# Kernel optimization log

Hardware: AMD Instinct MI355X
Metric: run time of the kernel (lower is better)

Reference implementation:

```python
import jax, jax.numpy as jnp
import numpy as np

B, T, E = 4, 2048, 1024
H, D = 16, 64  # num_heads, head_size; H*D == E


def setup_inputs() -> dict:
    key = jax.random.key(0)
    ks = jax.random.split(key, 8)
    s = 0.02
    x = jax.random.normal(ks[0], (B, T, E), dtype=jnp.float32)
    attention_mask = jnp.ones((B, T), dtype=jnp.float32)
    # stacked per-head projection weights (no bias), torch Linear: y = x @ W.T
    Wq = jax.random.normal(ks[1], (H, E, D), dtype=jnp.float32) * s
    Wk = jax.random.normal(ks[2], (H, E, D), dtype=jnp.float32) * s
    Wv = jax.random.normal(ks[3], (H, E, D), dtype=jnp.float32) * s
    Wo = jax.random.normal(ks[4], (E, E), dtype=jnp.float32) * s
    bo = jnp.zeros((E,), dtype=jnp.float32)
    return {"x": x, "attention_mask": attention_mask, "Wq": Wq, "Wk": Wk,
            "Wv": Wv, "Wo": Wo, "bo": bo}


def reference(x, attention_mask, Wq, Wk, Wv, Wo, bo):
    # per-head projections, vectorized over heads: [B,T,E] x [H,E,D] -> [B,H,T,D]
    q = jnp.einsum('bte,hed->bhtd', x, Wq)
    k = jnp.einsum('bte,hed->bhtd', x, Wk)
    v = jnp.einsum('bte,hed->bhtd', x, Wv)
    scores = jnp.einsum('bhtd,bhsd->bhts', q, k) / jnp.sqrt(jnp.float32(D))
    # causal mask (tril): masked_fill with -inf
    causal = jnp.tril(jnp.ones((T, T), dtype=bool))
    scores = jnp.where(causal[None, None, :, :], scores, -jnp.inf)
    # padding mask: weights += (1 - mask) * finfo(float32).min, broadcast over queries
    neg = jnp.finfo(jnp.float32).min
    scores = scores + ((1.0 - attention_mask) * neg)[:, None, None, :]
    weights = jax.nn.softmax(scores, axis=-1)
    out = jnp.einsum('bhts,bhsd->bthd', weights, v).reshape(B, T, H * D)
    return out @ Wo.T + bo
```

## Files before the change

### kernel.cpp

```cpp
#include <hip/hip_runtime.h>
#include <hip/hip_bf16.h>

#define B_ 4
#define T_ 2048
#define E_ 1024
#define H_ 16
#define D_ 64
#define M_ (B_*T_)

typedef short bf16x8 __attribute__((ext_vector_type(8)));
typedef float f32x4  __attribute__((ext_vector_type(4)));
typedef float f32x16 __attribute__((ext_vector_type(16)));

__device__ __forceinline__ short f2bf(float f) {
    __hip_bfloat16 h = __float2bfloat16(f);
    return *reinterpret_cast<short*>(&h);
}

__device__ __forceinline__ void async_ld16(const void* g, void* l) {
    __builtin_amdgcn_global_load_lds(
        (const __attribute__((address_space(1))) unsigned int*)g,
        (__attribute__((address_space(3))) unsigned int*)l, 16, 0, 0);
}

__global__ __launch_bounds__(256) void prep_fused(
        const float* __restrict__ x,   const float* __restrict__ Wo,
        const float* __restrict__ Wq,  const float* __restrict__ Wk,
        const float* __restrict__ Wv,  const float* __restrict__ mask,
        short* __restrict__ xb, short* __restrict__ Wob,
        short* __restrict__ Wt, float* __restrict__ bias) {
    __shared__ float tile[64][65];
    const int bi  = blockIdx.x;
    const int tid = threadIdx.x;

    if (bi < 9216) {
        const float* src = (bi < 8192) ? x : Wo;
        short* dst       = (bi < 8192) ? xb : Wob;
        const int i = ((bi < 8192) ? bi : (bi - 8192)) * 256 + tid;
        float4 v = ((const float4*)src)[i];
        short4 o = make_short4(f2bf(v.x), f2bf(v.y), f2bf(v.z), f2bf(v.w));
        ((short4*)dst)[i] = o;
    } else if (bi < 9984) {
        const int idx = bi - 9216;
        const int which = idx >> 8;
        const int h  = (idx & 255) >> 4;
        const int e0 = (idx & 15) * 64;
        const float* __restrict__ W = (which == 0) ? Wq : (which == 1) ? Wk : Wv;
#pragma unroll
        for (int r = 0; r < 4; ++r) {
            int lin = tid + r * 256;
            int er = lin >> 4, c4 = (lin & 15) * 4;
            float4 v = *(const float4*)(W + ((size_t)h * E_ + e0 + er) * D_ + c4);
            tile[er][c4 + 0] = v.x; tile[er][c4 + 1] = v.y;
            tile[er][c4 + 2] = v.z; tile[er][c4 + 3] = v.w;
        }
        __syncthreads();
#pragma unroll
        for (int r = 0; r < 4; ++r) {
            int lin = tid + r * 256;
            int dr = lin >> 4, j4 = (lin & 15) * 4;
            short4 o = make_short4(f2bf(tile[j4 + 0][dr]), f2bf(tile[j4 + 1][dr]),
                                   f2bf(tile[j4 + 2][dr]), f2bf(tile[j4 + 3][dr]));
            *(short4*)(Wt + ((size_t)which * 1024 + h * 64 + dr) * E_ + e0 + j4) = o;
        }
    } else {
        const int i = (bi - 9984) * 256 + tid;
        float bm = (1.0f - mask[i]) * -3.402823466e38f;
        bias[i] = fmaf(bm, 1.4426950f, -8.6561700f);
    }
}

template <int MODE>
__global__ __launch_bounds__(512, 4) void mfma_gemm(
        const short* __restrict__ A,
        const short* __restrict__ Bt,
        short* __restrict__ qo, short* __restrict__ ko, short* __restrict__ vo,
        float* __restrict__ Cout, const float* __restrict__ bo) {
    __shared__ __align__(16) char lds[3 * 24576];

    const int tid  = threadIdx.x;
    const int wave = tid >> 6, lane = tid & 63;
    const int c = lane & 15, quad = lane >> 4;
    const int wm = wave >> 1, wn = wave & 1;
    const int m0 = blockIdx.x * 256;
    const int n0 = blockIdx.y * 128;

    const int ar = tid >> 2;
    const int ag = (tid & 3) ^ ((tid >> 3) & 3);

    int aoff[4], boff[4];
#pragma unroll
    for (int mi = 0; mi < 4; ++mi) {
        int row = wm * 64 + mi * 16 + c;
        aoff[mi] = row * 64 + ((quad ^ ((row >> 1) & 3)) << 4);
    }
#pragma unroll
    for (int ni = 0; ni < 4; ++ni) {
        int row = wn * 64 + ni * 16 + c;
        boff[ni] = 16384 + row * 64 + ((quad ^ ((row >> 1) & 3)) << 4);
    }

    f32x4 acc[4][4] = {};

#define STG(bufb, k0v) do {                                                  \
        async_ld16(A  + (size_t)(m0 + ar) * 1024 + (k0v) + ag * 8,           \
                   lds + (bufb) + wave * 1024);                              \
        async_ld16(A  + (size_t)(m0 + 128 + ar) * 1024 + (k0v) + ag * 8,     \
                   lds + (bufb) + 8192 + wave * 1024);                       \
        async_ld16(Bt + (size_t)(n0 + ar) * 1024 + (k0v) + ag * 8,           \
                   lds + (bufb) + 16384 + wave * 1024);                      \
    } while (0)

    STG(0, 0);
    STG(24576, 32);
    asm volatile("s_waitcnt vmcnt(3)" ::: "memory");
    __builtin_amdgcn_s_barrier();

    int rbase = 0;
#pragma unroll 1
    for (int k = 0; k < 32; ++k) {
        const char* rb = lds + rbase;
        const int wbase = (rbase == 0) ? 49152 : rbase - 24576;

        if (k < 30) STG(wbase, (k + 2) * 32);

        bf16x8 a_[4], b_[4];
#pragma unroll
        for (int mi = 0; mi < 4; ++mi)
            a_[mi] = *(const bf16x8*)(rb + aoff[mi]);
#pragma unroll
        for (int ni = 0; ni < 4; ++ni)
            b_[ni] = *(const bf16x8*)(rb + boff[ni]);

        __builtin_amdgcn_s_setprio(1);
#pragma unroll
        for (int mi = 0; mi < 4; ++mi)
#pragma unroll
            for (int ni = 0; ni < 4; ++ni)
                acc[mi][ni] = __builtin_amdgcn_mfma_f32_16x16x32_bf16(
                    a_[mi], b_[ni], acc[mi][ni], 0, 0, 0);
        __builtin_amdgcn_s_setprio(0);

        if (k < 30)       asm volatile("s_waitcnt vmcnt(3)" ::: "memory");
        else if (k == 30) asm volatile("s_waitcnt vmcnt(0)" ::: "memory");
        if (k < 31) __builtin_amdgcn_s_barrier();

        rbase = (rbase == 49152) ? 0 : rbase + 24576;
    }
#undef STG

    if (MODE == 0) {
        const int which = n0 >> 10;
        const int nb = n0 & 1023;
        if (which == 2) {
#pragma unroll
            for (int mi = 0; mi < 4; ++mi) {
                const int m = m0 + wm * 64 + mi * 16 + quad * 4;
                const int b = m >> 11, t = m & 2047;
#pragma unroll
                for (int ni = 0; ni < 4; ++ni) {
                    const int n = nb + wn * 64 + ni * 16 + c;
                    const int h = n >> 6, d = n & 63;
                    short4 s4 = make_short4(f2bf(acc[mi][ni][0]), f2bf(acc[mi][ni][1]),
                                            f2bf(acc[mi][ni][2]), f2bf(acc[mi][ni][3]));
                    *(short4*)(vo + (((size_t)b * H_ + h) * D_ + d) * T_ + t) = s4;
                }
            }
        } else {
            short* __restrict__ outp = (which == 0) ? qo : ko;
            const float sc = (which == 0) ? 0.18033688f : 1.0f;
#pragma unroll
            for (int mi = 0; mi < 4; ++mi) {
#pragma unroll
                for (int i = 0; i < 4; ++i) {
                    const int m = m0 + wm * 64 + mi * 16 + quad * 4 + i;
                    const int b = m >> 11, t = m & 2047;
#pragma unroll
                    for (int ni = 0; ni < 4; ++ni) {
                        const int n = nb + wn * 64 + ni * 16 + c;
                        const int h = n >> 6, d = n & 63;
                        outp[(((size_t)b * H_ + h) * T_ + t) * D_ + d] =
                            f2bf(acc[mi][ni][i] * sc);
                    }
                }
            }
        }
    } else {
#pragma unroll
        for (int mi = 0; mi < 4; ++mi) {
#pragma unroll
            for (int i = 0; i < 4; ++i) {
                const int m = m0 + wm * 64 + mi * 16 + quad * 4 + i;
#pragma unroll
                for (int ni = 0; ni < 4; ++ni) {
                    const int n = n0 + wn * 64 + ni * 16 + c;
                    Cout[(size_t)m * E_ + n] = acc[mi][ni][i] + bo[n];
                }
            }
        }
    }
}

__device__ __forceinline__ void attn_tile(
        const int tt, const int mytile, const char* __restrict__ lds,
        const int ln, const int hi, const bf16x8* __restrict__ qf,
        const int4 ka4, const int4 va4,
        f32x16& O0, f32x16& O1, float& lacc) {
    if (tt > mytile) return;
    const int s0 = tt << 5;
    const int bb = (tt & 3) * 8192;
    const int ka[4] = {ka4.x, ka4.y, ka4.z, ka4.w};
    const int va[4] = {va4.x, va4.y, va4.z, va4.w};

    f32x4 b4[4];
#pragma unroll
    for (int g = 0; g < 4; ++g)
        b4[g] = *(const f32x4*)(lds + 32768 + (s0 + g * 8 + hi * 4) * 4);

    f32x16 S = {};
    __builtin_amdgcn_s_setprio(1);
#pragma unroll
    for (int kc = 0; kc < 4; ++kc) {
        bf16x8 kv = *(const bf16x8*)(lds + bb + ka[kc]);
        S = __builtin_amdgcn_mfma_f32_32x32x16_bf16(kv, qf[kc], S, 0, 0, 0);
    }
    __builtin_amdgcn_s_setprio(0);

    float p[16];
#pragma unroll
    for (int r = 0; r < 16; ++r) {
        float bb2 = ((const float*)&b4[r >> 2])[r & 3];
        p[r] = __builtin_amdgcn_exp2f(S[r] + bb2);
    }
    if (tt == mytile) {
#pragma unroll
        for (int r = 0; r < 16; ++r)
            if (((r & 3) + ((r >> 2) << 3) + (hi << 2)) > ln)
                p[r] = 0.0f;
    }
    {
        float t0 = (p[0] + p[1]) + (p[2] + p[3]);
        float t1 = (p[4] + p[5]) + (p[6] + p[7]);
        float t2s = (p[8] + p[9]) + (p[10] + p[11]);
        float t3 = (p[12] + p[13]) + (p[14] + p[15]);
        lacc += (t0 + t1) + (t2s + t3);
    }

    unsigned int u0, u1, u2, u3, u4, u5, u6, u7;
    asm("v_cvt_pk_bf16_f32 %0, %1, %2" : "=v"(u0) : "v"(p[0]),  "v"(p[1]));
    asm("v_cvt_pk_bf16_f32 %0, %1, %2" : "=v"(u1) : "v"(p[2]),  "v"(p[3]));
    asm("v_cvt_pk_bf16_f32 %0, %1, %2" : "=v"(u2) : "v"(p[4]),  "v"(p[5]));
    asm("v_cvt_pk_bf16_f32 %0, %1, %2" : "=v"(u3) : "v"(p[6]),  "v"(p[7]));
    asm("v_cvt_pk_bf16_f32 %0, %1, %2" : "=v"(u4) : "v"(p[8]),  "v"(p[9]));
    asm("v_cvt_pk_bf16_f32 %0, %1, %2" : "=v"(u5) : "v"(p[10]), "v"(p[11]));
    asm("v_cvt_pk_bf16_f32 %0, %1, %2" : "=v"(u6) : "v"(p[12]), "v"(p[13]));
    asm("v_cvt_pk_bf16_f32 %0, %1, %2" : "=v"(u7) : "v"(p[14]), "v"(p[15]));
    asm("v_permlane32_swap_b32 %0, %1" : "+v"(u0), "+v"(u2));
    asm("v_permlane32_swap_b32 %0, %1" : "+v"(u1), "+v"(u3));
    asm("v_permlane32_swap_b32 %0, %1" : "+v"(u4), "+v"(u6));
    asm("v_permlane32_swap_b32 %0, %1" : "+v"(u5), "+v"(u7));
    union { unsigned int w[4]; bf16x8 v; } pa0, pa1;
    pa0.w[0] = u0; pa0.w[1] = u1; pa0.w[2] = u2; pa0.w[3] = u3;
    pa1.w[0] = u4; pa1.w[1] = u5; pa1.w[2] = u6; pa1.w[3] = u7;

    bf16x8 v00 = *(const bf16x8*)(lds + bb + va[0]);
    bf16x8 v01 = *(const bf16x8*)(lds + bb + va[1]);
    bf16x8 v10 = *(const bf16x8*)(lds + bb + va[2]);
    bf16x8 v11 = *(const bf16x8*)(lds + bb + va[3]);
    __builtin_amdgcn_s_setprio(1);
    O0 = __builtin_amdgcn_mfma_f32_32x32x16_bf16(pa0.v, v00, O0, 0, 0, 0);
    O0 = __builtin_amdgcn_mfma_f32_32x32x16_bf16(pa1.v, v01, O0, 0, 0, 0);
    O1 = __builtin_amdgcn_mfma_f32_32x32x16_bf16(pa0.v, v10, O1, 0, 0, 0);
    O1 = __builtin_amdgcn_mfma_f32_32x32x16_bf16(pa1.v, v11, O1, 0, 0, 0);
    __builtin_amdgcn_s_setprio(0);
}

__global__ __launch_bounds__(256, 4) void flash_attn8(
        const short* __restrict__ qg,
        const short* __restrict__ kg,
        const short* __restrict__ vtg,
        const float* __restrict__ biasg,
        short* __restrict__ attn) {
    const int h = blockIdx.x, b = blockIdx.y;
    const int kb = 15 - blockIdx.z;
    const int tid  = threadIdx.x;
    const int wave = tid >> 6, lane = tid & 63;
    const int ln = lane & 31, hi = lane >> 5;
    const int q0w = kb * 128 + wave * 32;
    const int mytile = 4 * kb + wave;
    const int nt = 4 * kb + 4;
    const int np = nt >> 1;

    __shared__ __align__(16) char lds[40960];

    const size_t bh = (size_t)b * H_ + h;
    const short* qbh  = qg  + bh * (size_t)T_ * D_;
    const short* kbh  = kg  + bh * (size_t)T_ * D_;
    const short* vtbh = vtg + bh * (size_t)D_ * T_;
    const float* biasb = biasg + (size_t)b * T_;

    const int ks = tid >> 3, kgs = (tid & 7) ^ (ks & 7);
    const int vd = tid >> 2, vgs = ((tid & 3) - (vd >> 1)) & 3;

    int4 ka4, va4;
    {
        int tmp[4];
#pragma unroll
        for (int kc = 0; kc < 4; ++kc)
            tmp[kc] = ln * 128 + ((((kc << 1) + hi) ^ (ln & 7)) << 4);
        ka4 = make_int4(tmp[0], tmp[1], tmp[2], tmp[3]);
#pragma unroll
        for (int dh = 0; dh < 2; ++dh)
#pragma unroll
            for (int kc2 = 0; kc2 < 2; ++kc2) {
                int d = dh * 32 + ln;
                tmp[dh * 2 + kc2] =
                    4096 + d * 64 + (((((kc2 << 1) + hi) + (d >> 1)) & 3) << 4);
            }
        va4 = make_int4(tmp[0], tmp[1], tmp[2], tmp[3]);
    }

    bf16x8 qf[4];
#pragma unroll
    for (int kc = 0; kc < 4; ++kc)
        qf[kc] = *(const bf16x8*)(qbh + (size_t)(q0w + ln) * D_ + kc * 16 + hi * 8);

#pragma unroll
    for (int r = 0; r < 2; ++r)
        async_ld16(biasb + r * 1024 + tid * 4,
                   lds + 32768 + r * 4096 + wave * 1024);

#define STAGE_T(tt2) do {                                                   \
        const int _s0 = (tt2) << 5;                                         \
        const int _bb = ((tt2) & 3) * 8192;                                 \
        async_ld16(kbh + (size_t)(_s0 + ks) * D_ + (kgs << 3),              \
                   lds + _bb + wave * 1024);                                \
        async_ld16(vtbh + (size_t)vd * T_ + _s0 + (vgs << 3),               \
                   lds + _bb + 4096 + wave * 1024);                         \
    } while (0)

    STAGE_T(0);
    STAGE_T(1);

    f32x16 O0 = {}, O1 = {};
    float lacc = 0.0f;

#pragma unroll 1
    for (int j = 0; j < np; ++j) {
        asm volatile("s_waitcnt vmcnt(0)" ::: "memory");
        __builtin_amdgcn_s_barrier();
        if (j + 1 < np) { STAGE_T(2 * j + 2); STAGE_T(2 * j + 3); }

        attn_tile(2 * j,     mytile, lds, ln, hi, qf, ka4, va4, O0, O1, lacc);
        attn_tile(2 * j + 1, mytile, lds, ln, hi, qf, ka4, va4, O0, O1, lacc);
    }
#undef STAGE_T

    unsigned int la = __float_as_uint(lacc), lb2 = la;
    asm("v_permlane32_swap_b32 %0, %1" : "+v"(la), "+v"(lb2));
    const float ltot = __uint_as_float(la) + __uint_as_float(lb2);

    __syncthreads();
    float* lsh = (float*)lds + wave * 32;
    if (hi == 0) lsh[ln] = 1.0f / ltot;
    __syncthreads();

    short* ab = attn + (size_t)b * T_ * E_ + h * D_;
#pragma unroll
    for (int r = 0; r < 16; ++r) {
        const int qrow = (r & 3) + ((r >> 2) << 3) + (hi << 2);
        const float iv = lsh[qrow];
        const size_t base = (size_t)(q0w + qrow) * E_;
        ab[base + ln]      = f2bf(O0[r] * iv);
        ab[base + 32 + ln] = f2bf(O1[r] * iv);
    }
}

extern "C" void kernel_launch(void* const* d_in, const int* in_sizes, int n_in,
                              void* d_out, int out_size, void* d_ws, size_t ws_size,
                              hipStream_t stream) {
    const float* x    = (const float*)d_in[0];
    const float* mask = (const float*)d_in[1];
    const float* Wq   = (const float*)d_in[2];
    const float* Wk   = (const float*)d_in[3];
    const float* Wv   = (const float*)d_in[4];
    const float* Wo   = (const float*)d_in[5];
    const float* bo   = (const float*)d_in[6];
    float* out        = (float*)d_out;

    const size_t S = (size_t)M_ * E_;
    char* ws = (char*)d_ws;
    short* xb   = (short*)ws;
    short* qb   = (short*)(ws + S * 2);
    short* kb   = (short*)(ws + S * 4);
    short* vtb  = (short*)(ws + S * 6);
    short* Wt   = (short*)(ws + S * 8);
    short* Wob  = (short*)(ws + S * 8 + (size_t)3 * 1024 * 1024 * 2);
    float* bias = (float*)(ws + S * 8 + (size_t)4 * 1024 * 1024 * 2);
    short* attnb = xb;

    prep_fused<<<dim3(10016), 256, 0, stream>>>(
        x, Wo, Wq, Wk, Wv, mask, xb, Wob, Wt, bias);

    mfma_gemm<0><<<dim3(M_ / 256, 3 * E_ / 128), 512, 0, stream>>>(
        xb, Wt, qb, kb, vtb, nullptr, nullptr);

    flash_attn8<<<dim3(H_, B_, 16), 256, 0, stream>>>(qb, kb, vtb, bias, attnb);

    mfma_gemm<1><<<dim3(M_ / 256, E_ / 128), 512, 0, stream>>>(
        attnb, Wob, nullptr, nullptr, nullptr, out, bo);
}
```

Baseline: 230.3 us.

## Load GEMM A operand directly from global memory, stage only B in LDS

The A tile is no longer staged through shared memory. Each wave now reads its A fragments straight from global memory into registers every k-step, and only the B tile goes through the triple-buffered async LDS path. This cuts LDS use from 72KB to 24KB per block, which could allow more resident blocks and removes the A LDS writes and reads. The cost is that A is no longer prefetched, so its global latency sits on the critical path each iteration. The two waves sharing each A row also fetch it twice, and the vmcnt waits now count the A loads as well.

```diff
diff --git a/kernel.cpp b/kernel.cpp
--- a/kernel.cpp
+++ b/kernel.cpp
@@ -76,7 +76,7 @@
         const short* __restrict__ Bt,
         short* __restrict__ qo, short* __restrict__ ko, short* __restrict__ vo,
         float* __restrict__ Cout, const float* __restrict__ bo) {
-    __shared__ __align__(16) char lds[3 * 24576];
+    __shared__ __align__(16) char lds[3 * 8192];
 
     const int tid  = threadIdx.x;
     const int wave = tid >> 6, lane = tid & 63;
@@ -85,49 +85,44 @@
     const int m0 = blockIdx.x * 256;
     const int n0 = blockIdx.y * 128;
 
-    const int ar = tid >> 2;
-    const int ag = (tid & 3) ^ ((tid >> 3) & 3);
-
-    int aoff[4], boff[4];
-#pragma unroll
-    for (int mi = 0; mi < 4; ++mi) {
-        int row = wm * 64 + mi * 16 + c;
-        aoff[mi] = row * 64 + ((quad ^ ((row >> 1) & 3)) << 4);
-    }
+    const int br = tid >> 2;
+    const int bg = (tid & 3) ^ ((tid >> 3) & 3);
+
+    int boff[4];
 #pragma unroll
     for (int ni = 0; ni < 4; ++ni) {
         int row = wn * 64 + ni * 16 + c;
-        boff[ni] = 16384 + row * 64 + ((quad ^ ((row >> 1) & 3)) << 4);
-    }
+        boff[ni] = row * 64 + ((quad ^ ((row >> 1) & 3)) << 4);
+    }
+
+    const short* aptr[4];
+#pragma unroll
+    for (int mi = 0; mi < 4; ++mi)
+        aptr[mi] = A + (size_t)(m0 + wm * 64 + mi * 16 + c) * 1024 + quad * 8;
 
     f32x4 acc[4][4] = {};
 
-#define STG(bufb, k0v) do {                                                  \
-        async_ld16(A  + (size_t)(m0 + ar) * 1024 + (k0v) + ag * 8,           \
-                   lds + (bufb) + wave * 1024);                              \
-        async_ld16(A  + (size_t)(m0 + 128 + ar) * 1024 + (k0v) + ag * 8,     \
-                   lds + (bufb) + 8192 + wave * 1024);                       \
-        async_ld16(Bt + (size_t)(n0 + ar) * 1024 + (k0v) + ag * 8,           \
-                   lds + (bufb) + 16384 + wave * 1024);                      \
-    } while (0)
-
-    STG(0, 0);
-    STG(24576, 32);
-    asm volatile("s_waitcnt vmcnt(3)" ::: "memory");
+#define STGB(bufb, k0v)                                                      \
+    async_ld16(Bt + (size_t)(n0 + br) * 1024 + (k0v) + bg * 8,               \
+               lds + (bufb) + wave * 1024)
+
+    STGB(0, 0);
+    STGB(8192, 32);
+    asm volatile("s_waitcnt vmcnt(1)" ::: "memory");
     __builtin_amdgcn_s_barrier();
 
     int rbase = 0;
 #pragma unroll 1
     for (int k = 0; k < 32; ++k) {
         const char* rb = lds + rbase;
-        const int wbase = (rbase == 0) ? 49152 : rbase - 24576;
-
-        if (k < 30) STG(wbase, (k + 2) * 32);
+        const int wbase = (rbase == 0) ? 16384 : rbase - 8192;
+        if (k < 30) STGB(wbase, (k + 2) * 32);
 
         bf16x8 a_[4], b_[4];
+        const int ka = k * 32;
 #pragma unroll
         for (int mi = 0; mi < 4; ++mi)
-            a_[mi] = *(const bf16x8*)(rb + aoff[mi]);
+            a_[mi] = *(const bf16x8*)(aptr[mi] + ka);
 #pragma unroll
         for (int ni = 0; ni < 4; ++ni)
             b_[ni] = *(const bf16x8*)(rb + boff[ni]);
@@ -141,13 +136,13 @@
                     a_[mi], b_[ni], acc[mi][ni], 0, 0, 0);
         __builtin_amdgcn_s_setprio(0);
 
-        if (k < 30)       asm volatile("s_waitcnt vmcnt(3)" ::: "memory");
+        if (k < 30)       asm volatile("s_waitcnt vmcnt(1)" ::: "memory");
         else if (k == 30) asm volatile("s_waitcnt vmcnt(0)" ::: "memory");
         if (k < 31) __builtin_amdgcn_s_barrier();
 
-        rbase = (rbase == 49152) ? 0 : rbase + 24576;
-    }
-#undef STG
+        rbase = (rbase == 16384) ? 0 : rbase + 8192;
+    }
+#undef STGB
 
     if (MODE == 0) {
         const int which = n0 >> 10;
```

New measurement: 318.1 us. +38.1%, slower.
